# Kernel tuning notes

Hardware: AMD Instinct MI355X
Metric: run time of the kernel (lower is better)

Reference implementation:

```python
import jax, jax.numpy as jnp
import numpy as np

N_HEADS = 12
D_MODEL = 768
D_HEAD = 64
LN_EPS = 1e-5


def setup_inputs() -> dict:
    key = jax.random.key(0)
    ks = jax.random.split(key, 7)
    bs, slen = 1, 4096
    s_in = 1.0 / np.sqrt(D_MODEL)
    s_out = 1.0 / np.sqrt(N_HEADS * D_HEAD)
    return {
        "x": jax.random.normal(ks[0], (bs, slen, D_MODEL), jnp.float32),
        "W_attn": jax.random.uniform(ks[1], (D_MODEL, 3 * N_HEADS * D_HEAD), jnp.float32, -s_in, s_in),
        "b_attn": jax.random.uniform(ks[2], (3 * N_HEADS * D_HEAD,), jnp.float32, -s_in, s_in),
        "W_out": jax.random.uniform(ks[3], (N_HEADS * D_HEAD, D_MODEL), jnp.float32, -s_out, s_out),
        "b_out": jax.random.uniform(ks[4], (D_MODEL,), jnp.float32, -s_out, s_out),
        "ln_g": jnp.ones((D_MODEL,), jnp.float32),
        "ln_b": jnp.zeros((D_MODEL,), jnp.float32),
    }


def reference(x, W_attn, b_attn, W_out, b_out, ln_g, ln_b):
    bs, slen, _ = x.shape
    qkv = x @ W_attn + b_attn                      # [b, s, 3*H*D]
    wq, wk, wv = jnp.split(qkv, 3, axis=-1)
    def to_heads(t):
        return t.reshape(bs, slen, N_HEADS, D_HEAD)
    q, k, v = to_heads(wq), to_heads(wk), to_heads(wv)
    # scores: [b, h, s_q, s_k]
    scores = jnp.einsum('bqhd,bkhd->bhqk', q, k) / np.sqrt(D_HEAD).astype(np.float32)
    probs = jax.nn.softmax(scores, axis=-1)
    attn = jnp.einsum('bhqk,bkhd->bqhd', probs, v).reshape(bs, slen, N_HEADS * D_HEAD)
    out = attn @ W_out + b_out
    y = x + out
    mu = jnp.mean(y, axis=-1, keepdims=True)
    var = jnp.mean(jnp.square(y - mu), axis=-1, keepdims=True)
    return (y - mu) / jnp.sqrt(var + LN_EPS) * ln_g + ln_b
```

## Files before the change

### kernel.cpp

```cpp
#include <hip/hip_runtime.h>
#include <cstdint>
#include <cstddef>

#define SL 4096
#define DM 768

typedef short s16x8 __attribute__((ext_vector_type(8)));
typedef unsigned short u16x8 __attribute__((ext_vector_type(8)));
typedef unsigned short u16x4 __attribute__((ext_vector_type(4)));
typedef float f32x4 __attribute__((ext_vector_type(4)));
typedef float f32x16 __attribute__((ext_vector_type(16)));
typedef unsigned int u32x4 __attribute__((ext_vector_type(4)));

__device__ __forceinline__ unsigned short f2bf(float f) {
  unsigned u = __float_as_uint(f);
  u = u + 0x7fffu + ((u >> 16) & 1u);
  return (unsigned short)(u >> 16);
}

__device__ __forceinline__ int swz(int row, int col) {
  return (row << 6) + ((((col >> 3) ^ row) & 7) << 3) + (col & 7);
}

__device__ __forceinline__ int aswz(int row, int col) {
  return (row << 6) + ((((col >> 3) ^ row ^ (row >> 3)) & 7) << 3) + (col & 7);
}

__device__ __forceinline__ int vswz(int d, int col) {
  return (d << 5) + ((((col >> 3) ^ (d >> 1)) & 3) << 3) + (col & 7);
}

#define ASYNC16(G, L)                                                        \
  __builtin_amdgcn_global_load_lds(                                          \
      (const __attribute__((address_space(1))) void*)(G),                    \
      (__attribute__((address_space(3))) void*)(L), 16, 0, 0)

#define WAITB()                                   \
  do {                                            \
    asm volatile("s_waitcnt vmcnt(0)" ::: "memory"); \
    __builtin_amdgcn_s_barrier();                 \
  } while (0)

extern "C" __global__ __launch_bounds__(256) void k_cvt(
    const float* __restrict__ in, unsigned short* __restrict__ out, int n) {
  int i = (blockIdx.x * 256 + threadIdx.x) * 4;
  if (i >= n) return;
  f32x4 v = *reinterpret_cast<const f32x4*>(in + i);
  u16x4 o;
  o[0] = f2bf(v[0]); o[1] = f2bf(v[1]); o[2] = f2bf(v[2]); o[3] = f2bf(v[3]);
  *reinterpret_cast<u16x4*>(out + i) = o;
}

extern "C" __global__ __launch_bounds__(256) void k_tr(
    const float* __restrict__ in, unsigned short* __restrict__ out, int R, int C) {
  __shared__ float tile[64][65];
  const int t = threadIdx.x;
  const int r0 = blockIdx.y * 64, c0 = blockIdx.x * 64;
  const int lr = t >> 2, lcb = (t & 3) * 16;
  #pragma unroll
  for (int j = 0; j < 16; j += 4) {
    f32x4 v = *reinterpret_cast<const f32x4*>(in + (size_t)(r0 + lr) * C + c0 + lcb + j);
    tile[lr][lcb + j + 0] = v[0];
    tile[lr][lcb + j + 1] = v[1];
    tile[lr][lcb + j + 2] = v[2];
    tile[lr][lcb + j + 3] = v[3];
  }
  __syncthreads();
  #pragma unroll
  for (int j = 0; j < 16; j += 4) {
    u16x4 o;
    o[0] = f2bf(tile[lcb + j + 0][lr]);
    o[1] = f2bf(tile[lcb + j + 1][lr]);
    o[2] = f2bf(tile[lcb + j + 2][lr]);
    o[3] = f2bf(tile[lcb + j + 3][lr]);
    *reinterpret_cast<u16x4*>(out + (size_t)(c0 + lr) * R + r0 + lcb + j) = o;
  }
}

__device__ __forceinline__ void gemm_body(
    const unsigned short* al, const unsigned short* bl, f32x4* acc,
    int wv, int l15, int lg) {
  #pragma unroll
  for (int kc = 0; kc < 2; kc++) {
    s16x8 af = *reinterpret_cast<const s16x8*>(&al[swz(wv * 16 + l15, kc * 32 + lg * 8)]);
    #pragma unroll
    for (int nt = 0; nt < 4; nt++) {
      s16x8 bfr = *reinterpret_cast<const s16x8*>(&bl[swz(nt * 16 + l15, kc * 32 + lg * 8)]);
      acc[nt] = __builtin_amdgcn_mfma_f32_16x16x32_bf16(af, bfr, acc[nt], 0, 0, 0);
    }
  }
}

extern "C" __global__ __launch_bounds__(256) void k_qkv(
    const unsigned short* __restrict__ xbf, const unsigned short* __restrict__ wt,
    const float* __restrict__ bias, unsigned short* __restrict__ qb,
    unsigned short* __restrict__ kbo, unsigned short* __restrict__ vt) {
  __shared__ alignas(16) unsigned short a_lds[2][4096];
  __shared__ alignas(16) unsigned short b_lds[2][4096];
  const int t = threadIdx.x, wv = t >> 6, l = t & 63;
  const int l15 = l & 15, lg = l >> 4;
  const int m0 = blockIdx.y * 64, n0 = blockIdx.x * 64;
  f32x4 acc[4];
  acc[0] = acc[1] = acc[2] = acc[3] = (f32x4)0.f;
  int soff[2];
  #pragma unroll
  for (int c = 0; c < 2; c++) {
    int idx = wv * 128 + c * 64 + l;
    int row = idx >> 3, bp = idx & 7;
    int cb = (bp ^ row) & 7;
    soff[c] = row * DM + cb * 8;
  }
  const unsigned short* asrc = xbf + (size_t)m0 * DM;
  const unsigned short* bsrc = wt + (size_t)n0 * DM;
  unsigned short* la = &a_lds[0][0];
  unsigned short* lb = &b_lds[0][0];

#define STAGE_AB(B, KK)                                              \
  do {                                                               \
    ASYNC16(asrc + (KK) + soff[0], la + (B)*4096 + wv * 1024);       \
    ASYNC16(asrc + (KK) + soff[1], la + (B)*4096 + wv * 1024 + 512); \
    ASYNC16(bsrc + (KK) + soff[0], lb + (B)*4096 + wv * 1024);       \
    ASYNC16(bsrc + (KK) + soff[1], lb + (B)*4096 + wv * 1024 + 512); \
  } while (0)

  STAGE_AB(0, 0);
  WAITB();
  for (int kk = 0; kk < DM; kk += 128) {
    STAGE_AB(1, kk + 64);
    gemm_body(&a_lds[0][0], &b_lds[0][0], acc, wv, l15, lg);
    WAITB();
    if (kk + 128 < DM) STAGE_AB(0, kk + 128);
    gemm_body(&a_lds[1][0], &b_lds[1][0], acc, wv, l15, lg);
    WAITB();
  }
#undef STAGE_AB
  const int mb = m0 + wv * 16 + lg * 4;
  #pragma unroll
  for (int nt = 0; nt < 4; nt++) {
    const int n = n0 + nt * 16 + l15;
    const float bv = bias[n];
    const int sec = n / DM;
    const int nn = n - sec * DM;
    const int h = nn >> 6, d = nn & 63;
    if (sec == 0) {
      #pragma unroll
      for (int r = 0; r < 4; r++)
        qb[((size_t)h * SL + mb + r) * 64 + d] = f2bf((acc[nt][r] + bv) * 0.180336880f);
    } else if (sec == 1) {
      #pragma unroll
      for (int r = 0; r < 4; r++)
        kbo[((size_t)h * SL + mb + r) * 64 + d] = f2bf(acc[nt][r] + bv);
    } else {
      u16x4 o;
      #pragma unroll
      for (int r = 0; r < 4; r++) o[r] = f2bf(acc[nt][r] + bv);
      *reinterpret_cast<u16x4*>(vt + ((size_t)h * 64 + d) * SL + mb) = o;
    }
  }
}

extern "C" __global__ __launch_bounds__(256) void k_kmax(
    const unsigned short* __restrict__ kbf, unsigned* __restrict__ kmax) {
  const int h = blockIdx.x >> 4, part = blockIdx.x & 15;
  const unsigned short* row = kbf + ((size_t)h * SL + part * 256 + threadIdx.x) * 64;
  float ss = 0.f;
  #pragma unroll
  for (int j = 0; j < 64; j += 8) {
    u16x8 v = *reinterpret_cast<const u16x8*>(row + j);
    #pragma unroll
    for (int e = 0; e < 8; e++) {
      float f = __uint_as_float((unsigned)v[e] << 16);
      ss = fmaf(f, f, ss);
    }
  }
  #pragma unroll
  for (int off = 1; off < 64; off <<= 1) ss = fmaxf(ss, __shfl_xor(ss, off, 64));
  __shared__ float red[4];
  if ((threadIdx.x & 63) == 0) red[threadIdx.x >> 6] = ss;
  __syncthreads();
  if (threadIdx.x == 0) {
    float m = fmaxf(fmaxf(red[0], red[1]), fmaxf(red[2], red[3]));
    atomicMax(kmax + h, __float_as_uint(sqrtf(m)));
  }
}

extern "C" __global__ __launch_bounds__(256) void k_qbnd(
    const unsigned short* __restrict__ qbf, const unsigned* __restrict__ kmax,
    float* __restrict__ M) {
  const int idx = blockIdx.x * 256 + threadIdx.x;
  const unsigned short* row = qbf + (size_t)idx * 64;
  float ss = 0.f;
  #pragma unroll
  for (int j = 0; j < 64; j += 8) {
    u16x8 v = *reinterpret_cast<const u16x8*>(row + j);
    #pragma unroll
    for (int e = 0; e < 8; e++) {
      float f = __uint_as_float((unsigned)v[e] << 16);
      ss = fmaf(f, f, ss);
    }
  }
  M[idx] = sqrtf(ss) * __uint_as_float(kmax[idx >> 12]);
}

__device__ __forceinline__ void attn_body32f(
    const unsigned short* kb, const unsigned short* vb,
    const s16x8* qf, f32x16* ot, f32x16& lacc, float negM,
    const int* kfo, const int* vfo, s16x8 ones) {
  f32x16 st = (f32x16)0.f;
  __builtin_amdgcn_s_setprio(1);
  #pragma unroll
  for (int c = 0; c < 4; c++) {
    s16x8 kf = *reinterpret_cast<const s16x8*>(&kb[kfo[c]]);
    st = __builtin_amdgcn_mfma_f32_32x32x16_bf16(kf, qf[c], st, 0, 0, 0);
  }
  __builtin_amdgcn_s_setprio(0);
  #pragma unroll
  for (int r = 0; r < 16; r++) st[r] = exp2f(st[r] + negM);
  #pragma unroll
  for (int m = 0; m < 2; m++) {
    const int m0 = m * 8;
    unsigned w0, w1, w2, w3;
    asm("v_cvt_pk_bf16_f32 %0, %1, %2" : "=v"(w0) : "v"(st[m0 + 0]), "v"(st[m0 + 1]));
    asm("v_cvt_pk_bf16_f32 %0, %1, %2" : "=v"(w1) : "v"(st[m0 + 2]), "v"(st[m0 + 3]));
    asm("v_cvt_pk_bf16_f32 %0, %1, %2" : "=v"(w2) : "v"(st[m0 + 4]), "v"(st[m0 + 5]));
    asm("v_cvt_pk_bf16_f32 %0, %1, %2" : "=v"(w3) : "v"(st[m0 + 6]), "v"(st[m0 + 7]));
    asm volatile("v_permlane32_swap_b32 %0, %1" : "+v"(w0), "+v"(w2));
    asm volatile("v_permlane32_swap_b32 %0, %1" : "+v"(w1), "+v"(w3));
    u32x4 wv_;
    wv_[0] = w0; wv_[1] = w1; wv_[2] = w2; wv_[3] = w3;
    s16x8 pbf = *reinterpret_cast<s16x8*>(&wv_);
    __builtin_amdgcn_s_setprio(1);
    #pragma unroll
    for (int dt = 0; dt < 2; dt++) {
      s16x8 vf = *reinterpret_cast<const s16x8*>(&vb[vfo[m * 2 + dt]]);
      ot[dt] = __builtin_amdgcn_mfma_f32_32x32x16_bf16(vf, pbf, ot[dt], 0, 0, 0);
    }
    lacc = __builtin_amdgcn_mfma_f32_32x32x16_bf16(ones, pbf, lacc, 0, 0, 0);
    __builtin_amdgcn_s_setprio(0);
  }
}

extern "C" __global__ __launch_bounds__(256) void k_attn(
    const unsigned short* __restrict__ qb, const unsigned short* __restrict__ kbi,
    const unsigned short* __restrict__ vt, const float* __restrict__ Mb,
    unsigned short* __restrict__ aout) {
  __shared__ alignas(16) unsigned char smem[32768];
  unsigned short* kst = (unsigned short*)smem;
  unsigned short* vst = (unsigned short*)(smem + 16384);
  const int t = threadIdx.x, w = t >> 6, l = t & 63;
  const int l31 = l & 31, s = l >> 5;
  const int half = w >> 1, qs = w & 1;
  const int bid = blockIdx.x;
  const int sid = (bid & 7) * 96 + (bid >> 3);
  const int h = sid >> 6, qt = sid & 63;
  const unsigned short* qh = qb + (size_t)h * SL * 64;
  const unsigned short* kh = kbi + (size_t)h * SL * 64 + (size_t)half * 2048 * 64;
  const unsigned short* vh = vt + (size_t)h * 64 * SL + half * 2048;
  const int q = qt * 64 + qs * 32 + l31;
  const float negM = -Mb[h * SL + q];
  s16x8 qf[4];
  #pragma unroll
  for (int c = 0; c < 4; c++)
    qf[c] = *reinterpret_cast<const s16x8*>(qh + (size_t)q * 64 + c * 16 + s * 8);
  s16x8 ones;
  #pragma unroll
  for (int e = 0; e < 8; e++) ones[e] = (short)0x3F80;
  f32x16 ot[2];
  ot[0] = (f32x16)0.f;
  ot[1] = (f32x16)0.f;
  f32x16 lacc = (f32x16)0.f;
  int koff[2], voff[2];
  #pragma unroll
  for (int c = 0; c < 2; c++) {
    int i = (qs * 2 + c) * 64 + l;
    int key = i >> 3, kb_ = i & 7;
    koff[c] = key * 64 + (kb_ ^ ((key ^ (key >> 3)) & 7)) * 8;
    int d = i >> 2, vb_ = i & 3;
    voff[c] = d * SL + (vb_ ^ ((d >> 1) & 3)) * 8;
  }
  int kfo[4], vfo[4];
  #pragma unroll
  for (int c = 0; c < 4; c++) kfo[c] = aswz(l31, c * 16 + s * 8);
  #pragma unroll
  for (int m = 0; m < 2; m++)
    #pragma unroll
    for (int dt = 0; dt < 2; dt++) vfo[m * 2 + dt] = vswz(dt * 32 + l31, m * 16 + s * 8);

#define STAGE_KV(B, LB)                                                     \
  do {                                                                      \
    _Pragma("unroll")                                                       \
    for (int c = 0; c < 2; c++) {                                           \
      ASYNC16(kh + (size_t)(LB) * 64 + koff[c],                             \
              kst + (half * 2 + (B)) * 2048 + (qs * 2 + c) * 512);          \
      ASYNC16(vh + (LB) + voff[c],                                          \
              vst + (half * 2 + (B)) * 2048 + (qs * 2 + c) * 512);          \
    }                                                                       \
  } while (0)

  STAGE_KV(0, 0);
  WAITB();
  for (int lb = 0; lb < 2048; lb += 64) {
    STAGE_KV(1, lb + 32);
    attn_body32f(kst + (half * 2) * 2048, vst + (half * 2) * 2048,
                 qf, ot, lacc, negM, kfo, vfo, ones);
    WAITB();
    if (lb + 64 < 2048) STAGE_KV(0, lb + 64);
    attn_body32f(kst + (half * 2 + 1) * 2048, vst + (half * 2 + 1) * 2048,
                 qf, ot, lacc, negM, kfo, vfo, ones);
    WAITB();
  }
#undef STAGE_KV
  const float lsum = lacc[0];
  float* o_m = (float*)smem;
  float* l_m = (float*)(smem + 17408);
  __syncthreads();
  if (half == 1) {
    #pragma unroll
    for (int dt = 0; dt < 2; dt++) {
      #pragma unroll
      for (int rq = 0; rq < 4; rq++) {
        f32x4 v;
        #pragma unroll
        for (int j = 0; j < 4; j++) v[j] = ot[dt][rq * 4 + j];
        *reinterpret_cast<f32x4*>(&o_m[(qs * 32 + l31) * 68 + dt * 32 + rq * 8 + s * 4]) = v;
      }
    }
    if (s == 0) l_m[qs * 32 + l31] = lsum;
  }
  __syncthreads();
  if (half == 0) {
    const float linv = 1.f / (lsum + l_m[qs * 32 + l31]);
    #pragma unroll
    for (int dt = 0; dt < 2; dt++) {
      #pragma unroll
      for (int rq = 0; rq < 4; rq++) {
        f32x4 vb_ = *reinterpret_cast<const f32x4*>(&o_m[(qs * 32 + l31) * 68 + dt * 32 + rq * 8 + s * 4]);
        u16x4 o;
        #pragma unroll
        for (int j = 0; j < 4; j++)
          o[j] = f2bf((ot[dt][rq * 4 + j] + vb_[j]) * linv);
        *reinterpret_cast<u16x4*>(aout + (size_t)q * DM + h * 64 + dt * 32 + rq * 8 + s * 4) = o;
      }
    }
  }
}

extern "C" __global__ __launch_bounds__(256) void k_out(
    const unsigned short* __restrict__ abf, const unsigned short* __restrict__ wot,
    const float* __restrict__ bias, const float* __restrict__ x, float* __restrict__ y) {
  __shared__ alignas(16) unsigned short a_lds[2][4096];
  __shared__ alignas(16) unsigned short b_lds[2][4096];
  const int t = threadIdx.x, wv = t >> 6, l = t & 63;
  const int l15 = l & 15, lg = l >> 4;
  const int m0 = blockIdx.y * 64, n0 = blockIdx.x * 64;
  f32x4 acc[4];
  acc[0] = acc[1] = acc[2] = acc[3] = (f32x4)0.f;
  int soff[2];
  #pragma unroll
  for (int c = 0; c < 2; c++) {
    int idx = wv * 128 + c * 64 + l;
    int row = idx >> 3, bp = idx & 7;
    int cb = (bp ^ row) & 7;
    soff[c] = row * DM + cb * 8;
  }
  const unsigned short* asrc = abf + (size_t)m0 * DM;
  const unsigned short* bsrc = wot + (size_t)n0 * DM;
  unsigned short* la = &a_lds[0][0];
  unsigned short* lb = &b_lds[0][0];

#define STAGE_AB(B, KK)                                              \
  do {                                                               \
    ASYNC16(asrc + (KK) + soff[0], la + (B)*4096 + wv * 1024);       \
    ASYNC16(asrc + (KK) + soff[1], la + (B)*4096 + wv * 1024 + 512); \
    ASYNC16(bsrc + (KK) + soff[0], lb + (B)*4096 + wv * 1024);       \
    ASYNC16(bsrc + (KK) + soff[1], lb + (B)*4096 + wv * 1024 + 512); \
  } while (0)

  STAGE_AB(0, 0);
  WAITB();
  for (int kk = 0; kk < DM; kk += 128) {
    STAGE_AB(1, kk + 64);
    gemm_body(&a_lds[0][0], &b_lds[0][0], acc, wv, l15, lg);
    WAITB();
    if (kk + 128 < DM) STAGE_AB(0, kk + 128);
    gemm_body(&a_lds[1][0], &b_lds[1][0], acc, wv, l15, lg);
    WAITB();
  }
#undef STAGE_AB
  const int mb = m0 + wv * 16 + lg * 4;
  #pragma unroll
  for (int nt = 0; nt < 4; nt++) {
    const int n = n0 + nt * 16 + l15;
    const float bv = bias[n];
    #pragma unroll
    for (int r = 0; r < 4; r++)
      y[(size_t)(mb + r) * DM + n] = acc[nt][r] + bv + x[(size_t)(mb + r) * DM + n];
  }
}

extern "C" __global__ __launch_bounds__(256) void k_ln(
    const float* __restrict__ y, const float* __restrict__ g, const float* __restrict__ b,
    float* __restrict__ out) {
  const int row = blockIdx.x, t = threadIdx.x;
  const float* yr = y + (size_t)row * DM;
  float v0 = yr[t], v1 = yr[t + 256], v2 = yr[t + 512];
  float sum = v0 + v1 + v2;
  float sq = v0 * v0 + v1 * v1 + v2 * v2;
  #pragma unroll
  for (int off = 1; off < 64; off <<= 1) {
    sum += __shfl_xor(sum, off, 64);
    sq += __shfl_xor(sq, off, 64);
  }
  __shared__ float ls[8];
  const int wv = t >> 6, l = t & 63;
  if (l == 0) { ls[wv] = sum; ls[4 + wv] = sq; }
  __syncthreads();
  sum = ls[0] + ls[1] + ls[2] + ls[3];
  sq = ls[4] + ls[5] + ls[6] + ls[7];
  const float mu = sum * (1.f / DM);
  const float rstd = rsqrtf(sq * (1.f / DM) - mu * mu + 1e-5f);
  out[(size_t)row * DM + t] = (v0 - mu) * rstd * g[t] + b[t];
  out[(size_t)row * DM + t + 256] = (v1 - mu) * rstd * g[t + 256] + b[t + 256];
  out[(size_t)row * DM + t + 512] = (v2 - mu) * rstd * g[t + 512] + b[t + 512];
}

extern "C" void kernel_launch(void* const* d_in, const int* in_sizes, int n_in,
                              void* d_out, int out_size, void* d_ws, size_t ws_size,
                              hipStream_t stream) {
  (void)in_sizes; (void)n_in; (void)out_size; (void)ws_size;
  const float* x = (const float*)d_in[0];
  const float* Wa = (const float*)d_in[1];
  const float* ba = (const float*)d_in[2];
  const float* Wo = (const float*)d_in[3];
  const float* bo = (const float*)d_in[4];
  const float* lng = (const float*)d_in[5];
  const float* lnb = (const float*)d_in[6];
  float* out = (float*)d_out;

  unsigned short* ws16 = (unsigned short*)d_ws;
  unsigned short* xbf = ws16;
  unsigned short* wat = xbf + 3145728;
  unsigned short* wot = wat + 1769472;
  unsigned short* qbf = wot + 589824;
  unsigned short* kbf = qbf + 3145728;
  unsigned short* vtb = kbf + 3145728;
  unsigned short* aob = vtb + 3145728;
  float* ybuf = (float*)(aob + 3145728);
  float* Mb = ybuf + 3145728;
  unsigned* kmx = (unsigned*)(Mb + 49152);

  hipMemsetAsync(kmx, 0, 12 * sizeof(unsigned), stream);
  k_cvt<<<3072, 256, 0, stream>>>(x, xbf, 3145728);
  k_tr<<<dim3(36, 12), 256, 0, stream>>>(Wa, wat, 768, 2304);
  k_tr<<<dim3(12, 12), 256, 0, stream>>>(Wo, wot, 768, 768);
  k_qkv<<<dim3(36, 64), 256, 0, stream>>>(xbf, wat, ba, qbf, kbf, vtb);
  k_kmax<<<192, 256, 0, stream>>>(kbf, kmx);
  k_qbnd<<<192, 256, 0, stream>>>(qbf, kmx, Mb);
  k_attn<<<768, 256, 0, stream>>>(qbf, kbf, vtb, Mb, aob);
  k_out<<<dim3(12, 64), 256, 0, stream>>>(aob, wot, bo, x, ybuf);
  k_ln<<<4096, 256, 0, stream>>>(ybuf, lng, lnb, out);
}
```

Before: 180.6 us.

## Fuse prep kernels, enlarge QKV tiles, fold norm bounds into QKV epilogue

Merges the bf16 convert, both weight transposes and the kmax reset into one prep launch. Enlarges the QKV GEMM block tile to 128x128 with 4x4 MFMA tiles per wave, and computes q squared norms and the per-head k max norm in its epilogue, which removes the separate kmax and qbnd kernels. The attention kernel now subtracts the softmax bound through an extra MFMA with a bf16-rounded -M instead of a per-element add. This cuts launches and memory passes, but raises register and LDS use in the QKV kernel and rounds the bound to bf16.

```diff
diff --git a/kernel.cpp b/kernel.cpp
--- a/kernel.cpp
+++ b/kernel.cpp
@@ -41,21 +41,10 @@
     __builtin_amdgcn_s_barrier();                 \
   } while (0)
 
-extern "C" __global__ __launch_bounds__(256) void k_cvt(
-    const float* __restrict__ in, unsigned short* __restrict__ out, int n) {
-  int i = (blockIdx.x * 256 + threadIdx.x) * 4;
-  if (i >= n) return;
-  f32x4 v = *reinterpret_cast<const f32x4*>(in + i);
-  u16x4 o;
-  o[0] = f2bf(v[0]); o[1] = f2bf(v[1]); o[2] = f2bf(v[2]); o[3] = f2bf(v[3]);
-  *reinterpret_cast<u16x4*>(out + i) = o;
-}
-
-extern "C" __global__ __launch_bounds__(256) void k_tr(
-    const float* __restrict__ in, unsigned short* __restrict__ out, int R, int C) {
-  __shared__ float tile[64][65];
-  const int t = threadIdx.x;
-  const int r0 = blockIdx.y * 64, c0 = blockIdx.x * 64;
+__device__ __forceinline__ void tr_body(
+    const float* __restrict__ in, unsigned short* __restrict__ out,
+    int R, int C, int bx, int by, float (*tile)[65], int t) {
+  const int r0 = by * 64, c0 = bx * 64;
   const int lr = t >> 2, lcb = (t & 3) * 16;
   #pragma unroll
   for (int j = 0; j < 16; j += 4) {
@@ -77,134 +66,198 @@
   }
 }
 
-__device__ __forceinline__ void gemm_body(
-    const unsigned short* al, const unsigned short* bl, f32x4* acc,
-    int wv, int l15, int lg) {
-  #pragma unroll
-  for (int kc = 0; kc < 2; kc++) {
-    s16x8 af = *reinterpret_cast<const s16x8*>(&al[swz(wv * 16 + l15, kc * 32 + lg * 8)]);
-    #pragma unroll
-    for (int nt = 0; nt < 4; nt++) {
-      s16x8 bfr = *reinterpret_cast<const s16x8*>(&bl[swz(nt * 16 + l15, kc * 32 + lg * 8)]);
-      acc[nt] = __builtin_amdgcn_mfma_f32_16x16x32_bf16(af, bfr, acc[nt], 0, 0, 0);
-    }
+extern "C" __global__ __launch_bounds__(256) void k_prep(
+    const float* __restrict__ x, const float* __restrict__ Wa,
+    const float* __restrict__ Wo, unsigned short* __restrict__ xbf,
+    unsigned short* __restrict__ wat, unsigned short* __restrict__ wot,
+    unsigned* __restrict__ kmx) {
+  __shared__ float tile[64][65];
+  const int b = blockIdx.x, t = threadIdx.x;
+  if (b < 3072) {
+    if (b == 0 && t < 12) kmx[t] = 0u;
+    const int i = (b * 256 + t) * 4;
+    f32x4 v = *reinterpret_cast<const f32x4*>(x + i);
+    u16x4 o;
+    o[0] = f2bf(v[0]); o[1] = f2bf(v[1]); o[2] = f2bf(v[2]); o[3] = f2bf(v[3]);
+    *reinterpret_cast<u16x4*>(xbf + i) = o;
+  } else if (b < 3504) {
+    const int bb = b - 3072;
+    tr_body(Wa, wat, 768, 2304, bb % 36, bb / 36, tile, t);
+  } else {
+    const int bb = b - 3504;
+    tr_body(Wo, wot, 768, 768, bb % 12, bb / 12, tile, t);
   }
 }
 
 extern "C" __global__ __launch_bounds__(256) void k_qkv(
     const unsigned short* __restrict__ xbf, const unsigned short* __restrict__ wt,
     const float* __restrict__ bias, unsigned short* __restrict__ qb,
-    unsigned short* __restrict__ kbo, unsigned short* __restrict__ vt) {
-  __shared__ alignas(16) unsigned short a_lds[2][4096];
-  __shared__ alignas(16) unsigned short b_lds[2][4096];
-  const int t = threadIdx.x, wv = t >> 6, l = t & 63;
+    unsigned short* __restrict__ kbo, unsigned short* __restrict__ vtb,
+    float* __restrict__ qn2, unsigned* __restrict__ kmx) {
+  __shared__ alignas(16) unsigned short a_lds[2][8192];
+  __shared__ alignas(16) unsigned short b_lds[2][8192];
+  const int t = threadIdx.x, w = t >> 6, l = t & 63;
   const int l15 = l & 15, lg = l >> 4;
-  const int m0 = blockIdx.y * 64, n0 = blockIdx.x * 64;
-  f32x4 acc[4];
-  acc[0] = acc[1] = acc[2] = acc[3] = (f32x4)0.f;
-  int soff[2];
-  #pragma unroll
-  for (int c = 0; c < 2; c++) {
-    int idx = wv * 128 + c * 64 + l;
-    int row = idx >> 3, bp = idx & 7;
-    int cb = (bp ^ row) & 7;
-    soff[c] = row * DM + cb * 8;
+  const int wr = w >> 1, wc = w & 1;
+  const int n0 = blockIdx.x * 128, m0 = blockIdx.y * 128;
+  f32x4 acc[4][4];
+  #pragma unroll
+  for (int mt = 0; mt < 4; mt++)
+    #pragma unroll
+    for (int nt = 0; nt < 4; nt++) acc[mt][nt] = (f32x4)0.f;
+  int soff[4];
+  #pragma unroll
+  for (int c = 0; c < 4; c++) {
+    int i = c * 256 + t;
+    int row = i >> 3, bp = i & 7;
+    soff[c] = row * DM + (bp ^ (row & 7)) * 8;
   }
   const unsigned short* asrc = xbf + (size_t)m0 * DM;
   const unsigned short* bsrc = wt + (size_t)n0 * DM;
-  unsigned short* la = &a_lds[0][0];
-  unsigned short* lb = &b_lds[0][0];
-
-#define STAGE_AB(B, KK)                                              \
-  do {                                                               \
-    ASYNC16(asrc + (KK) + soff[0], la + (B)*4096 + wv * 1024);       \
-    ASYNC16(asrc + (KK) + soff[1], la + (B)*4096 + wv * 1024 + 512); \
-    ASYNC16(bsrc + (KK) + soff[0], lb + (B)*4096 + wv * 1024);       \
-    ASYNC16(bsrc + (KK) + soff[1], lb + (B)*4096 + wv * 1024 + 512); \
+
+#define STAGE128(B, KK)                                                   \
+  do {                                                                    \
+    _Pragma("unroll")                                                     \
+    for (int c = 0; c < 4; c++) {                                         \
+      ASYNC16(asrc + (KK) + soff[c], &a_lds[B][0] + c * 2048 + w * 512);  \
+      ASYNC16(bsrc + (KK) + soff[c], &b_lds[B][0] + c * 2048 + w * 512);  \
+    }                                                                     \
   } while (0)
 
-  STAGE_AB(0, 0);
+#define GEMM128(B)                                                            \
+  do {                                                                        \
+    _Pragma("unroll")                                                         \
+    for (int kc = 0; kc < 2; kc++) {                                          \
+      s16x8 af[4], bfv[4];                                                    \
+      _Pragma("unroll")                                                       \
+      for (int mt = 0; mt < 4; mt++)                                          \
+        af[mt] = *reinterpret_cast<const s16x8*>(                             \
+            &a_lds[B][swz(wr * 64 + mt * 16 + l15, kc * 32 + lg * 8)]);       \
+      _Pragma("unroll")                                                       \
+      for (int nt = 0; nt < 4; nt++)                                          \
+        bfv[nt] = *reinterpret_cast<const s16x8*>(                            \
+            &b_lds[B][swz(wc * 64 + nt * 16 + l15, kc * 32 + lg * 8)]);       \
+      _Pragma("unroll")                                                       \
+      for (int mt = 0; mt < 4; mt++)                                          \
+        _Pragma("unroll")                                                     \
+        for (int nt = 0; nt < 4; nt++)                                        \
+          acc[mt][nt] = __builtin_amdgcn_mfma_f32_16x16x32_bf16(              \
+              af[mt], bfv[nt], acc[mt][nt], 0, 0, 0);                         \
+    }                                                                         \
+  } while (0)
+
+  STAGE128(0, 0);
   WAITB();
+  #pragma unroll 1
   for (int kk = 0; kk < DM; kk += 128) {
-    STAGE_AB(1, kk + 64);
-    gemm_body(&a_lds[0][0], &b_lds[0][0], acc, wv, l15, lg);
+    STAGE128(1, kk + 64);
+    GEMM128(0);
     WAITB();
-    if (kk + 128 < DM) STAGE_AB(0, kk + 128);
-    gemm_body(&a_lds[1][0], &b_lds[1][0], acc, wv, l15, lg);
+    if (kk + 128 < DM) STAGE128(0, kk + 128);
+    GEMM128(1);
     WAITB();
   }
-#undef STAGE_AB
-  const int mb = m0 + wv * 16 + lg * 4;
-  #pragma unroll
-  for (int nt = 0; nt < 4; nt++) {
-    const int n = n0 + nt * 16 + l15;
-    const float bv = bias[n];
-    const int sec = n / DM;
-    const int nn = n - sec * DM;
-    const int h = nn >> 6, d = nn & 63;
-    if (sec == 0) {
-      #pragma unroll
-      for (int r = 0; r < 4; r++)
-        qb[((size_t)h * SL + mb + r) * 64 + d] = f2bf((acc[nt][r] + bv) * 0.180336880f);
-    } else if (sec == 1) {
-      #pragma unroll
-      for (int r = 0; r < 4; r++)
-        kbo[((size_t)h * SL + mb + r) * 64 + d] = f2bf(acc[nt][r] + bv);
-    } else {
-      u16x4 o;
-      #pragma unroll
-      for (int r = 0; r < 4; r++) o[r] = f2bf(acc[nt][r] + bv);
-      *reinterpret_cast<u16x4*>(vt + ((size_t)h * 64 + d) * SL + mb) = o;
-    }
-  }
-}
-
-extern "C" __global__ __launch_bounds__(256) void k_kmax(
-    const unsigned short* __restrict__ kbf, unsigned* __restrict__ kmax) {
-  const int h = blockIdx.x >> 4, part = blockIdx.x & 15;
-  const unsigned short* row = kbf + ((size_t)h * SL + part * 256 + threadIdx.x) * 64;
-  float ss = 0.f;
-  #pragma unroll
-  for (int j = 0; j < 64; j += 8) {
-    u16x8 v = *reinterpret_cast<const u16x8*>(row + j);
-    #pragma unroll
-    for (int e = 0; e < 8; e++) {
-      float f = __uint_as_float((unsigned)v[e] << 16);
-      ss = fmaf(f, f, ss);
-    }
-  }
-  #pragma unroll
-  for (int off = 1; off < 64; off <<= 1) ss = fmaxf(ss, __shfl_xor(ss, off, 64));
-  __shared__ float red[4];
-  if ((threadIdx.x & 63) == 0) red[threadIdx.x >> 6] = ss;
-  __syncthreads();
-  if (threadIdx.x == 0) {
-    float m = fmaxf(fmaxf(red[0], red[1]), fmaxf(red[2], red[3]));
-    atomicMax(kmax + h, __float_as_uint(sqrtf(m)));
-  }
-}
-
-extern "C" __global__ __launch_bounds__(256) void k_qbnd(
-    const unsigned short* __restrict__ qbf, const unsigned* __restrict__ kmax,
-    float* __restrict__ M) {
-  const int idx = blockIdx.x * 256 + threadIdx.x;
-  const unsigned short* row = qbf + (size_t)idx * 64;
-  float ss = 0.f;
-  #pragma unroll
-  for (int j = 0; j < 64; j += 8) {
-    u16x8 v = *reinterpret_cast<const u16x8*>(row + j);
-    #pragma unroll
-    for (int e = 0; e < 8; e++) {
-      float f = __uint_as_float((unsigned)v[e] << 16);
-      ss = fmaf(f, f, ss);
-    }
-  }
-  M[idx] = sqrtf(ss) * __uint_as_float(kmax[idx >> 12]);
+#undef STAGE128
+#undef GEMM128
+
+  const int secn = (n0 >= 1536) ? 2 : (n0 >= 768 ? 1 : 0);
+  const int nbase = n0 - secn * 768 + wc * 64;
+  const int h = nbase >> 6;
+  const int mrow0 = m0 + wr * 64;
+  float bv4[4];
+  #pragma unroll
+  for (int nt = 0; nt < 4; nt++) bv4[nt] = bias[secn * 768 + nbase + nt * 16 + l15];
+
+  if (secn == 0) {
+    const float QS = 0.180336880f;
+    float s2[4][4];
+    #pragma unroll
+    for (int mt = 0; mt < 4; mt++) {
+      #pragma unroll
+      for (int r = 0; r < 4; r++) s2[mt][r] = 0.f;
+    }
+    #pragma unroll
+    for (int mt = 0; mt < 4; mt++) {
+      #pragma unroll
+      for (int nt = 0; nt < 4; nt++) {
+        const int d = nt * 16 + l15;
+        #pragma unroll
+        for (int r = 0; r < 4; r++) {
+          const int m = mrow0 + mt * 16 + lg * 4 + r;
+          float v = (acc[mt][nt][r] + bv4[nt]) * QS;
+          qb[((size_t)h * SL + m) * 64 + d] = f2bf(v);
+          s2[mt][r] = fmaf(v, v, s2[mt][r]);
+        }
+      }
+    }
+    #pragma unroll
+    for (int mt = 0; mt < 4; mt++)
+      #pragma unroll
+      for (int r = 0; r < 4; r++) {
+        #pragma unroll
+        for (int off = 1; off < 16; off <<= 1)
+          s2[mt][r] += __shfl_xor(s2[mt][r], off, 64);
+      }
+    if (l15 == 0) {
+      #pragma unroll
+      for (int mt = 0; mt < 4; mt++)
+        #pragma unroll
+        for (int r = 0; r < 4; r++)
+          qn2[(size_t)h * SL + mrow0 + mt * 16 + lg * 4 + r] = s2[mt][r];
+    }
+  } else if (secn == 1) {
+    float s2[4][4];
+    #pragma unroll
+    for (int mt = 0; mt < 4; mt++) {
+      #pragma unroll
+      for (int r = 0; r < 4; r++) s2[mt][r] = 0.f;
+    }
+    #pragma unroll
+    for (int mt = 0; mt < 4; mt++) {
+      #pragma unroll
+      for (int nt = 0; nt < 4; nt++) {
+        const int d = nt * 16 + l15;
+        #pragma unroll
+        for (int r = 0; r < 4; r++) {
+          const int m = mrow0 + mt * 16 + lg * 4 + r;
+          float v = acc[mt][nt][r] + bv4[nt];
+          kbo[((size_t)h * SL + m) * 64 + d] = f2bf(v);
+          s2[mt][r] = fmaf(v, v, s2[mt][r]);
+        }
+      }
+    }
+    float rm = 0.f;
+    #pragma unroll
+    for (int mt = 0; mt < 4; mt++)
+      #pragma unroll
+      for (int r = 0; r < 4; r++) {
+        #pragma unroll
+        for (int off = 1; off < 16; off <<= 1)
+          s2[mt][r] += __shfl_xor(s2[mt][r], off, 64);
+        rm = fmaxf(rm, s2[mt][r]);
+      }
+    rm = fmaxf(rm, __shfl_xor(rm, 16, 64));
+    rm = fmaxf(rm, __shfl_xor(rm, 32, 64));
+    if (l == 0) atomicMax(kmx + h, __float_as_uint(rm));
+  } else {
+    #pragma unroll
+    for (int mt = 0; mt < 4; mt++) {
+      #pragma unroll
+      for (int nt = 0; nt < 4; nt++) {
+        const int d = nt * 16 + l15;
+        u16x4 o;
+        #pragma unroll
+        for (int r = 0; r < 4; r++) o[r] = f2bf(acc[mt][nt][r] + bv4[nt]);
+        *reinterpret_cast<u16x4*>(
+            vtb + ((size_t)h * 64 + d) * SL + mrow0 + mt * 16 + lg * 4) = o;
+      }
+    }
+  }
 }
 
 __device__ __forceinline__ void attn_body32f(
     const unsigned short* kb, const unsigned short* vb,
-    const s16x8* qf, f32x16* ot, f32x16& lacc, float negM,
+    const s16x8* qf, f32x16* ot, f32x16& lacc, s16x8 qm,
     const int* kfo, const int* vfo, s16x8 ones) {
   f32x16 st = (f32x16)0.f;
   __builtin_amdgcn_s_setprio(1);
@@ -213,9 +266,10 @@
     s16x8 kf = *reinterpret_cast<const s16x8*>(&kb[kfo[c]]);
     st = __builtin_amdgcn_mfma_f32_32x32x16_bf16(kf, qf[c], st, 0, 0, 0);
   }
+  st = __builtin_amdgcn_mfma_f32_32x32x16_bf16(ones, qm, st, 0, 0, 0);
   __builtin_amdgcn_s_setprio(0);
   #pragma unroll
-  for (int r = 0; r < 16; r++) st[r] = exp2f(st[r] + negM);
+  for (int r = 0; r < 16; r++) st[r] = exp2f(st[r]);
   #pragma unroll
   for (int m = 0; m < 2; m++) {
     const int m0 = m * 8;
@@ -242,8 +296,8 @@
 
 extern "C" __global__ __launch_bounds__(256) void k_attn(
     const unsigned short* __restrict__ qb, const unsigned short* __restrict__ kbi,
-    const unsigned short* __restrict__ vt, const float* __restrict__ Mb,
-    unsigned short* __restrict__ aout) {
+    const unsigned short* __restrict__ vt, const float* __restrict__ qn2,
+    const unsigned* __restrict__ kmx, unsigned short* __restrict__ aout) {
   __shared__ alignas(16) unsigned char smem[32768];
   unsigned short* kst = (unsigned short*)smem;
   unsigned short* vst = (unsigned short*)(smem + 16384);
@@ -257,7 +311,7 @@
   const unsigned short* kh = kbi + (size_t)h * SL * 64 + (size_t)half * 2048 * 64;
   const unsigned short* vh = vt + (size_t)h * 64 * SL + half * 2048;
   const int q = qt * 64 + qs * 32 + l31;
-  const float negM = -Mb[h * SL + q];
+  const float M = sqrtf(qn2[(size_t)h * SL + q] * __uint_as_float(kmx[h]));
   s16x8 qf[4];
   #pragma unroll
   for (int c = 0; c < 4; c++)
@@ -265,6 +319,8 @@
   s16x8 ones;
   #pragma unroll
   for (int e = 0; e < 8; e++) ones[e] = (short)0x3F80;
+  s16x8 qm = (s16x8)0;
+  if (s == 0) qm[0] = (short)f2bf(-M);
   f32x16 ot[2];
   ot[0] = (f32x16)0.f;
   ot[1] = (f32x16)0.f;
@@ -302,11 +358,11 @@
   for (int lb = 0; lb < 2048; lb += 64) {
     STAGE_KV(1, lb + 32);
     attn_body32f(kst + (half * 2) * 2048, vst + (half * 2) * 2048,
-                 qf, ot, lacc, negM, kfo, vfo, ones);
+                 qf, ot, lacc, qm, kfo, vfo, ones);
     WAITB();
     if (lb + 64 < 2048) STAGE_KV(0, lb + 64);
     attn_body32f(kst + (half * 2 + 1) * 2048, vst + (half * 2 + 1) * 2048,
-                 qf, ot, lacc, negM, kfo, vfo, ones);
+                 qf, ot, lacc, qm, kfo, vfo, ones);
     WAITB();
   }
 #undef STAGE_KV
@@ -341,6 +397,20 @@
           o[j] = f2bf((ot[dt][rq * 4 + j] + vb_[j]) * linv);
         *reinterpret_cast<u16x4*>(aout + (size_t)q * DM + h * 64 + dt * 32 + rq * 8 + s * 4) = o;
       }
+    }
+  }
+}
+
+__device__ __forceinline__ void gemm_body(
+    const unsigned short* al, const unsigned short* bl, f32x4* acc,
+    int wv, int l15, int lg) {
+  #pragma unroll
+  for (int kc = 0; kc < 2; kc++) {
+    s16x8 af = *reinterpret_cast<const s16x8*>(&al[swz(wv * 16 + l15, kc * 32 + lg * 8)]);
+    #pragma unroll
+    for (int nt = 0; nt < 4; nt++) {
+      s16x8 bfr = *reinterpret_cast<const s16x8*>(&bl[swz(nt * 16 + l15, kc * 32 + lg * 8)]);
+      acc[nt] = __builtin_amdgcn_mfma_f32_16x16x32_bf16(af, bfr, acc[nt], 0, 0, 0);
     }
   }
 }
@@ -360,8 +430,7 @@
   for (int c = 0; c < 2; c++) {
     int idx = wv * 128 + c * 64 + l;
     int row = idx >> 3, bp = idx & 7;
-    int cb = (bp ^ row) & 7;
-    soff[c] = row * DM + cb * 8;
+    soff[c] = row * DM + (bp ^ (row & 7)) * 8;
   }
   const unsigned short* asrc = abf + (size_t)m0 * DM;
   const unsigned short* bsrc = wot + (size_t)n0 * DM;
@@ -446,17 +515,12 @@
   unsigned short* vtb = kbf + 3145728;
   unsigned short* aob = vtb + 3145728;
   float* ybuf = (float*)(aob + 3145728);
-  float* Mb = ybuf + 3145728;
-  unsigned* kmx = (unsigned*)(Mb + 49152);
-
-  hipMemsetAsync(kmx, 0, 12 * sizeof(unsigned), stream);
-  k_cvt<<<3072, 256, 0, stream>>>(x, xbf, 3145728);
-  k_tr<<<dim3(36, 12), 256, 0, stream>>>(Wa, wat, 768, 2304);
-  k_tr<<<dim3(12, 12), 256, 0, stream>>>(Wo, wot, 768, 768);
-  k_qkv<<<dim3(36, 64), 256, 0, stream>>>(xbf, wat, ba, qbf, kbf, vtb);
-  k_kmax<<<192, 256, 0, stream>>>(kbf, kmx);
-  k_qbnd<<<192, 256, 0, stream>>>(qbf, kmx, Mb);
-  k_attn<<<768, 256, 0, stream>>>(qbf, kbf, vtb, Mb, aob);
+  float* qn2 = ybuf + 3145728;
+  unsigned* kmx = (unsigned*)(qn2 + 49152);
+
+  k_prep<<<3648, 256, 0, stream>>>(x, Wa, Wo, xbf, wat, wot, kmx);
+  k_qkv<<<dim3(18, 32), 256, 0, stream>>>(xbf, wat, ba, qbf, kbf, vtb, qn2, kmx);
+  k_attn<<<768, 256, 0, stream>>>(qbf, kbf, vtb, qn2, kmx, aob);
   k_out<<<dim3(12, 64), 256, 0, stream>>>(aob, wot, bo, x, ybuf);
   k_ln<<<4096, 256, 0, stream>>>(ybuf, lng, lnb, out);
 }
```

After: 165.2 us. 1.09x faster.
